# Kernel optimization log

Measured on AMD Instinct MI355X. Metric: run time of the kernel, lower is better.

## Reference

```python
import jax, jax.numpy as jnp
import numpy as np
from jax import lax

MAX_ALPHA = 0.00015
MAX_BETA = 0.00015
NOISE_GRAIN = 0.05
LN_EPS = 1e-5


def gaussian_blur(x, ksize, sigma):
    # depthwise 2D gaussian blur, same padding; x: [B, C, H, W]
    r = ksize // 2
    g = jnp.exp(-(jnp.linspace(-r, r, ksize, dtype=x.dtype) ** 2) / (2.0 * sigma ** 2))
    g = g / g.sum()
    k2d = g[:, None] * g[None, :]                       # [k, k]
    C = x.shape[1]
    kernel = jnp.broadcast_to(k2d, (C, 1, ksize, ksize))  # OIHW, depthwise
    return lax.conv_general_dilated(
        x, kernel, window_strides=(1, 1), padding=[(r, r), (r, r)],
        feature_group_count=C, dimension_numbers=('NCHW', 'OIHW', 'NCHW'))


def setup_inputs() -> dict:
    key = jax.random.key(0)
    ks = jax.random.split(key, 8)
    B, C, H, W = 8, 3, 1024, 1024
    L, D = 1024, 512
    Dh = D // 4
    return {
        'x_bg': jax.random.uniform(ks[0], (B, C, H, W), dtype=jnp.float32),
        'bottleneck_feat': jax.random.normal(ks[1], (B, L, D), dtype=jnp.float32),
        'mask': jax.random.uniform(ks[2], (B, 1, H, W), dtype=jnp.float32),
        'noise': jax.random.normal(ks[3], (B, C, H, W), dtype=jnp.float32),
        'W1': jax.random.normal(ks[4], (D, Dh), dtype=jnp.float32) * (1.0 / np.sqrt(D)),
        'b1': jnp.zeros((Dh,), dtype=jnp.float32),
        'ln_g': jnp.ones((Dh,), dtype=jnp.float32),
        'ln_b': jnp.zeros((Dh,), dtype=jnp.float32),
        'W2': jax.random.normal(ks[5], (Dh, 2), dtype=jnp.float32) * 0.01,
        'b2': jnp.zeros((2,), dtype=jnp.float32),
    }


def reference(x_bg, bottleneck_feat, mask, noise, W1, b1, ln_g, ln_b, W2, b2):
    # param head on global-pooled bottleneck feature
    feat_global = bottleneck_feat.mean(axis=1)                 # [B, D]
    h = feat_global @ W1 + b1                                  # [B, D/4]
    mu = h.mean(axis=-1, keepdims=True)
    var = ((h - mu) ** 2).mean(axis=-1, keepdims=True)
    h = (h - mu) * lax.rsqrt(var + LN_EPS) * ln_g + ln_b
    h = jax.nn.relu(h)
    params = h @ W2 + b2                                       # [B, 2]
    alpha = jax.nn.sigmoid(params[:, 0])[:, None, None, None] * MAX_ALPHA
    beta = jax.nn.sigmoid(params[:, 1])[:, None, None, None] * MAX_BETA

    # synthesize
    variance = alpha * x_bg + beta
    sigma = jnp.sqrt(jnp.maximum(variance, 1e-7))
    n = gaussian_blur(noise, 7, NOISE_GRAIN) * 1.5
    mask_soft = gaussian_blur(mask, 21, 5.0)                   # [B,1,H,W] broadcast
    noisy_output = x_bg + n * sigma * mask_soft
    return noisy_output, alpha, beta
```

## Files before the change

kernel.cpp:

```cpp
#include <hip/hip_runtime.h>
#include <math.h>

#define B 8
#define C 3
#define H 1024
#define W 1024
#define L 1024
#define D 512
#define DH 128
#define NPIX (H * W)
#define NOISY_ELEMS (B * C * NPIX)
#define TH 16

typedef float vf2 __attribute__((ext_vector_type(2)));
typedef float vf4 __attribute__((ext_vector_type(4)));

struct BlurW { float w[21]; };

__global__ __launch_bounds__(256) void hblur_colsum_kernel(
        const float* __restrict__ mask, float* __restrict__ hmask,
        const float* __restrict__ feat, float* __restrict__ partial, BlurW kw) {
    int wgid = blockIdx.x;
    int t = threadIdx.x;
    __shared__ float srow[W + 24];

    if (wgid < 8192) {
        int l = wgid;
        const float* src = mask + (size_t)l * W;
        if (t < 10) { srow[2 + t] = 0.f; srow[12 + W + t] = 0.f; }
        vf4 v = __builtin_nontemporal_load((const vf4*)src + t);
        ((vf4*)(srow + 12))[t] = v;
        __syncthreads();
        float* dst = hmask + (size_t)l * W;
        #pragma unroll
        for (int i = 0; i < 4; ++i) {
            int x = t + 256 * i;
            float acc = 0.f;
            #pragma unroll
            for (int k = 0; k < 10; ++k)
                acc = fmaf(kw.w[k], srow[x + 2 + k] + srow[x + 22 - k], acc);
            acc = fmaf(kw.w[10], srow[x + 12], acc);
            dst[x] = acc;
        }
    } else {
        int blk = wgid - 8192;
        int b = blk >> 6, chunk = blk & 63;
        const float* base = feat + (size_t)b * (L * D) + (size_t)chunk * 16 * D;
        float s0 = 0.f, s1 = 0.f;
        for (int ll = 0; ll < 16; ++ll) {
            s0 += base[ll * D + t];
            s1 += base[ll * D + t + 256];
        }
        float* dst = partial + (size_t)blk * D;
        dst[t] = s0;
        dst[t + 256] = s1;
    }
}

__global__ void head_kernel(const float* __restrict__ partial,
                            const float* __restrict__ W1, const float* __restrict__ b1,
                            const float* __restrict__ ln_g, const float* __restrict__ ln_b,
                            const float* __restrict__ W2, const float* __restrict__ b2,
                            float* __restrict__ ab, float* __restrict__ out_tail) {
    const int b = blockIdx.x;
    const int j = threadIdx.x;
    __shared__ float fm[D];
    __shared__ float red[DH];
    for (int d = j; d < D; d += DH) {
        float s = 0.f;
        const float* p = partial + (size_t)b * 64 * D + d;
        for (int c = 0; c < 64; ++c) s += p[c * D];
        fm[d] = s * (1.0f / (float)L);
    }
    __syncthreads();
    float h = b1[j];
    const vf4* fm4 = (const vf4*)fm;
    #pragma unroll 8
    for (int d4 = 0; d4 < D / 4; ++d4) {
        vf4 f = fm4[d4];
        h = fmaf(f.x, W1[(4 * d4 + 0) * DH + j], h);
        h = fmaf(f.y, W1[(4 * d4 + 1) * DH + j], h);
        h = fmaf(f.z, W1[(4 * d4 + 2) * DH + j], h);
        h = fmaf(f.w, W1[(4 * d4 + 3) * DH + j], h);
    }

    red[j] = h; __syncthreads();
    for (int s = 64; s > 0; s >>= 1) { if (j < s) red[j] += red[j + s]; __syncthreads(); }
    float mu = red[0] * (1.f / (float)DH);
    __syncthreads();
    float hc = h - mu;
    red[j] = hc * hc; __syncthreads();
    for (int s = 64; s > 0; s >>= 1) { if (j < s) red[j] += red[j + s]; __syncthreads(); }
    float var = red[0] * (1.f / (float)DH);
    __syncthreads();

    float hn = hc * rsqrtf(var + 1e-5f) * ln_g[j] + ln_b[j];
    hn = fmaxf(hn, 0.f);

    red[j] = hn * W2[j * 2 + 0]; __syncthreads();
    for (int s = 64; s > 0; s >>= 1) { if (j < s) red[j] += red[j + s]; __syncthreads(); }
    float p0 = red[0];
    __syncthreads();
    red[j] = hn * W2[j * 2 + 1]; __syncthreads();
    for (int s = 64; s > 0; s >>= 1) { if (j < s) red[j] += red[j + s]; __syncthreads(); }
    float p1 = red[0];

    if (j == 0) {
        float a  = 0.00015f / (1.f + expf(-(p0 + b2[0])));
        float be = 0.00015f / (1.f + expf(-(p1 + b2[1])));
        ab[b] = a; ab[8 + b] = be;
        out_tail[b] = a; out_tail[8 + b] = be;
    }
}

__global__ __launch_bounds__(256) void final_kernel(
        const float* __restrict__ x_bg, const float* __restrict__ noise,
        const float* __restrict__ hmask, const float* __restrict__ ab,
        float* __restrict__ out, BlurW kw) {
    int blk = blockIdx.x;
    int b   = blk >> 7;
    int rem = blk & 127;
    int s   = rem >> 1;
    int wj  = rem & 1;
    int h0  = s * TH;
    int t   = threadIdx.x;
    int x0  = wj * 512 + 2 * t;

    const float* hmb = hmask + (size_t)b * NPIX + x0;
    const vf2 zero2 = {0.f, 0.f};

    vf2 win[21];
    #pragma unroll
    for (int k = 0; k < 21; ++k) {
        int hy = h0 - 10 + k;
        win[k] = (hy >= 0 && hy < H) ? *(const vf2*)(hmb + (size_t)hy * W) : zero2;
    }

    float alpha = ab[b], beta = ab[8 + b];

    #pragma unroll
    for (int r = 0; r < TH; ++r) {
        vf2 ms = zero2;
        #pragma unroll
        for (int k = 0; k < 10; ++k) {
            float wk = kw.w[k];
            vf2 v1 = win[(r + k) % 21];
            vf2 v2 = win[(r + 20 - k) % 21];
            ms.x = fmaf(wk, v1.x + v2.x, ms.x);
            ms.y = fmaf(wk, v1.y + v2.y, ms.y);
        }
        {
            vf2 vm = win[(r + 10) % 21];
            ms.x = fmaf(kw.w[10], vm.x, ms.x);
            ms.y = fmaf(kw.w[10], vm.y, ms.y);
        }
        int h = h0 + r;
        #pragma unroll
        for (int c = 0; c < C; ++c) {
            size_t idx = (((size_t)(b * C + c) * H) + h) * W + x0;
            vf2 x = __builtin_nontemporal_load((const vf2*)(x_bg + idx));
            vf2 nz = __builtin_nontemporal_load((const vf2*)(noise + idx));
            vf2 o;
            float sgx = sqrtf(fmaxf(fmaf(alpha, x.x, beta), 1e-7f));
            float sgy = sqrtf(fmaxf(fmaf(alpha, x.y, beta), 1e-7f));
            o.x = fmaf(1.5f * nz.x * sgx, ms.x, x.x);
            o.y = fmaf(1.5f * nz.y * sgy, ms.y, x.y);
            __builtin_nontemporal_store(o, (vf2*)(out + idx));
        }
        if (r < TH - 1) {
            int hy = h0 + r + 11;
            win[r % 21] = (hy < H) ? *(const vf2*)(hmb + (size_t)hy * W) : zero2;
        }
    }
}

extern "C" void kernel_launch(void* const* d_in, const int* in_sizes, int n_in,
                              void* d_out, int out_size, void* d_ws, size_t ws_size,
                              hipStream_t stream) {
    const float* x_bg = (const float*)d_in[0];
    const float* feat = (const float*)d_in[1];
    const float* mask = (const float*)d_in[2];
    const float* noise = (const float*)d_in[3];
    const float* W1 = (const float*)d_in[4];
    const float* b1 = (const float*)d_in[5];
    const float* ln_g = (const float*)d_in[6];
    const float* ln_b = (const float*)d_in[7];
    const float* W2 = (const float*)d_in[8];
    const float* b2 = (const float*)d_in[9];
    float* out = (float*)d_out;

    float* ws_f = (float*)d_ws;
    float* partial = ws_f;
    float* ab = ws_f + 262144;
    float* hmask = ws_f + 262144 + 64;

    BlurW kw;
    {
        double g[21], s = 0.0;
        for (int i = 0; i < 21; ++i) { double x = (double)(i - 10); g[i] = exp(-x * x / 50.0); s += g[i]; }
        for (int i = 0; i < 21; ++i) kw.w[i] = (float)(g[i] / s);
    }

    hblur_colsum_kernel<<<8192 + 512, 256, 0, stream>>>(mask, hmask, feat, partial, kw);
    head_kernel<<<B, 128, 0, stream>>>(partial, W1, b1, ln_g, ln_b, W2, b2,
                                       ab, out + NOISY_ELEMS);
    final_kernel<<<B * 64 * 2, 256, 0, stream>>>(x_bg, noise, hmask, ab, out, kw);
}
```

Baseline: 104.7 us.

## Batch mask rows per block, vectorize blurs, and restructure final kernel accumulation

```diff
diff --git a/kernel.cpp b/kernel.cpp
--- a/kernel.cpp
+++ b/kernel.cpp
@@ -11,6 +11,8 @@
 #define NPIX (H * W)
 #define NOISY_ELEMS (B * C * NPIX)
 #define TH 16
+#define RPB 8
+#define LROW 1056
 
 typedef float vf2 __attribute__((ext_vector_type(2)));
 typedef float vf4 __attribute__((ext_vector_type(4)));
@@ -22,38 +24,57 @@
         const float* __restrict__ feat, float* __restrict__ partial, BlurW kw) {
     int wgid = blockIdx.x;
     int t = threadIdx.x;
-    __shared__ float srow[W + 24];
-
-    if (wgid < 8192) {
-        int l = wgid;
-        const float* src = mask + (size_t)l * W;
-        if (t < 10) { srow[2 + t] = 0.f; srow[12 + W + t] = 0.f; }
-        vf4 v = __builtin_nontemporal_load((const vf4*)src + t);
-        ((vf4*)(srow + 12))[t] = v;
+    __shared__ float Ls[RPB][LROW];
+
+    if (wgid < 1024) {
+        size_t row0 = (size_t)wgid * RPB;
+        const float* src = mask + row0 * W;
+        #pragma unroll
+        for (int r = 0; r < RPB; ++r) {
+            vf4 v = __builtin_nontemporal_load((const vf4*)(src + (size_t)r * W) + t);
+            *(vf4*)&Ls[r][12 + 4 * t] = v;
+        }
+        if (t < RPB * 10) {
+            int r = t / 10, i = t - 10 * r;
+            Ls[r][2 + i] = 0.f;
+            Ls[r][12 + W + i] = 0.f;
+        }
         __syncthreads();
-        float* dst = hmask + (size_t)l * W;
-        #pragma unroll
-        for (int i = 0; i < 4; ++i) {
-            int x = t + 256 * i;
-            float acc = 0.f;
+        float* dst = hmask + row0 * W;
+        #pragma unroll
+        for (int r = 0; r < RPB; ++r) {
+            float v[28];
             #pragma unroll
-            for (int k = 0; k < 10; ++k)
-                acc = fmaf(kw.w[k], srow[x + 2 + k] + srow[x + 22 - k], acc);
-            acc = fmaf(kw.w[10], srow[x + 12], acc);
-            dst[x] = acc;
+            for (int j = 0; j < 7; ++j) {
+                vf4 q = *(const vf4*)&Ls[r][4 * t + 4 * j];
+                v[4 * j] = q.x; v[4 * j + 1] = q.y; v[4 * j + 2] = q.z; v[4 * j + 3] = q.w;
+            }
+            vf4 o;
+            #pragma unroll
+            for (int i = 0; i < 4; ++i) {
+                float acc = 0.f;
+                #pragma unroll
+                for (int k = 0; k < 10; ++k)
+                    acc = fmaf(kw.w[k], v[i + 2 + k] + v[i + 22 - k], acc);
+                o[i] = fmaf(kw.w[10], v[i + 12], acc);
+            }
+            __builtin_nontemporal_store(o, (vf4*)(dst + (size_t)r * W) + t);
         }
     } else {
-        int blk = wgid - 8192;
-        int b = blk >> 6, chunk = blk & 63;
-        const float* base = feat + (size_t)b * (L * D) + (size_t)chunk * 16 * D;
-        float s0 = 0.f, s1 = 0.f;
+        int blk = wgid - 1024;
+        int b = blk >> 5, chunk = blk & 31;
+        int d4 = (t & 127) * 4;
+        int half = t >> 7;
+        const float* base = feat + (size_t)b * (L * D)
+                          + (size_t)(chunk * 32 + half * 16) * D + d4;
+        vf4 s = {0.f, 0.f, 0.f, 0.f};
+        #pragma unroll
         for (int ll = 0; ll < 16; ++ll) {
-            s0 += base[ll * D + t];
-            s1 += base[ll * D + t + 256];
-        }
-        float* dst = partial + (size_t)blk * D;
-        dst[t] = s0;
-        dst[t + 256] = s1;
+            vf4 v = *(const vf4*)(base + (size_t)ll * D);
+            s.x += v.x; s.y += v.y; s.z += v.z; s.w += v.w;
+        }
+        float* dst = partial + ((size_t)(b * 64 + chunk * 2 + half)) * 512 + d4;
+        *(vf4*)dst = s;
     }
 }
 
@@ -129,47 +150,41 @@
     const float* hmb = hmask + (size_t)b * NPIX + x0;
     const vf2 zero2 = {0.f, 0.f};
 
-    vf2 win[21];
+    vf2 ms[TH];
     #pragma unroll
-    for (int k = 0; k < 21; ++k) {
+    for (int r = 0; r < TH; ++r) ms[r] = zero2;
+
+    #pragma unroll
+    for (int k = 0; k < TH + 20; ++k) {
         int hy = h0 - 10 + k;
-        win[k] = (hy >= 0 && hy < H) ? *(const vf2*)(hmb + (size_t)hy * W) : zero2;
+        vf2 wv = (hy >= 0 && hy < H) ? *(const vf2*)(hmb + (size_t)hy * W) : zero2;
+        #pragma unroll
+        for (int r = 0; r < TH; ++r) {
+            int dk = k - r;
+            if (dk >= 0 && dk < 21) {
+                ms[r].x = fmaf(kw.w[dk], wv.x, ms[r].x);
+                ms[r].y = fmaf(kw.w[dk], wv.y, ms[r].y);
+            }
+        }
     }
 
     float alpha = ab[b], beta = ab[8 + b];
 
     #pragma unroll
-    for (int r = 0; r < TH; ++r) {
-        vf2 ms = zero2;
-        #pragma unroll
-        for (int k = 0; k < 10; ++k) {
-            float wk = kw.w[k];
-            vf2 v1 = win[(r + k) % 21];
-            vf2 v2 = win[(r + 20 - k) % 21];
-            ms.x = fmaf(wk, v1.x + v2.x, ms.x);
-            ms.y = fmaf(wk, v1.y + v2.y, ms.y);
-        }
-        {
-            vf2 vm = win[(r + 10) % 21];
-            ms.x = fmaf(kw.w[10], vm.x, ms.x);
-            ms.y = fmaf(kw.w[10], vm.y, ms.y);
-        }
-        int h = h0 + r;
-        #pragma unroll
-        for (int c = 0; c < C; ++c) {
-            size_t idx = (((size_t)(b * C + c) * H) + h) * W + x0;
-            vf2 x = __builtin_nontemporal_load((const vf2*)(x_bg + idx));
-            vf2 nz = __builtin_nontemporal_load((const vf2*)(noise + idx));
+    for (int c = 0; c < C; ++c) {
+        const float* xb = x_bg  + (((size_t)(b * C + c) * H) + h0) * W + x0;
+        const float* nb = noise + (((size_t)(b * C + c) * H) + h0) * W + x0;
+        float*       ob = out   + (((size_t)(b * C + c) * H) + h0) * W + x0;
+        #pragma unroll
+        for (int r = 0; r < TH; ++r) {
+            vf2 x  = __builtin_nontemporal_load((const vf2*)(xb + (size_t)r * W));
+            vf2 nz = __builtin_nontemporal_load((const vf2*)(nb + (size_t)r * W));
             vf2 o;
             float sgx = sqrtf(fmaxf(fmaf(alpha, x.x, beta), 1e-7f));
             float sgy = sqrtf(fmaxf(fmaf(alpha, x.y, beta), 1e-7f));
-            o.x = fmaf(1.5f * nz.x * sgx, ms.x, x.x);
-            o.y = fmaf(1.5f * nz.y * sgy, ms.y, x.y);
-            __builtin_nontemporal_store(o, (vf2*)(out + idx));
-        }
-        if (r < TH - 1) {
-            int hy = h0 + r + 11;
-            win[r % 21] = (hy < H) ? *(const vf2*)(hmb + (size_t)hy * W) : zero2;
+            o.x = fmaf(1.5f * nz.x * sgx, ms[r].x, x.x);
+            o.y = fmaf(1.5f * nz.y * sgy, ms[r].y, x.y);
+            *(vf2*)(ob + (size_t)r * W) = o;
         }
     }
 }
@@ -201,7 +216,7 @@
         for (int i = 0; i < 21; ++i) kw.w[i] = (float)(g[i] / s);
     }
 
-    hblur_colsum_kernel<<<8192 + 512, 256, 0, stream>>>(mask, hmask, feat, partial, kw);
+    hblur_colsum_kernel<<<1024 + 256, 256, 0, stream>>>(mask, hmask, feat, partial, kw);
     head_kernel<<<B, 128, 0, stream>>>(partial, W1, b1, ln_g, ln_b, W2, b2,
                                        ab, out + NOISY_ELEMS);
     final_kernel<<<B * 64 * 2, 256, 0, stream>>>(x_bg, noise, hmask, ab, out, kw);
```

Result: faster. 100.8 us (-3.7%).

## Fuse mask blur into final kernel and merge colsum with head via atomic counter

Applied to the files above, without the earlier changes.

```diff
diff --git a/kernel.cpp b/kernel.cpp
--- a/kernel.cpp
+++ b/kernel.cpp
@@ -17,80 +17,61 @@
 
 struct BlurW { float w[21]; };
 
-__global__ __launch_bounds__(256) void hblur_colsum_kernel(
-        const float* __restrict__ mask, float* __restrict__ hmask,
-        const float* __restrict__ feat, float* __restrict__ partial, BlurW kw) {
-    int wgid = blockIdx.x;
-    int t = threadIdx.x;
-    __shared__ float srow[W + 24];
-
-    if (wgid < 8192) {
-        int l = wgid;
-        const float* src = mask + (size_t)l * W;
-        if (t < 10) { srow[2 + t] = 0.f; srow[12 + W + t] = 0.f; }
-        vf4 v = __builtin_nontemporal_load((const vf4*)src + t);
-        ((vf4*)(srow + 12))[t] = v;
-        __syncthreads();
-        float* dst = hmask + (size_t)l * W;
-        #pragma unroll
-        for (int i = 0; i < 4; ++i) {
-            int x = t + 256 * i;
-            float acc = 0.f;
-            #pragma unroll
-            for (int k = 0; k < 10; ++k)
-                acc = fmaf(kw.w[k], srow[x + 2 + k] + srow[x + 22 - k], acc);
-            acc = fmaf(kw.w[10], srow[x + 12], acc);
-            dst[x] = acc;
-        }
-    } else {
-        int blk = wgid - 8192;
-        int b = blk >> 6, chunk = blk & 63;
-        const float* base = feat + (size_t)b * (L * D) + (size_t)chunk * 16 * D;
-        float s0 = 0.f, s1 = 0.f;
-        for (int ll = 0; ll < 16; ++ll) {
-            s0 += base[ll * D + t];
-            s1 += base[ll * D + t + 256];
-        }
-        float* dst = partial + (size_t)blk * D;
-        dst[t] = s0;
-        dst[t + 256] = s1;
-    }
-}
-
-__global__ void head_kernel(const float* __restrict__ partial,
-                            const float* __restrict__ W1, const float* __restrict__ b1,
-                            const float* __restrict__ ln_g, const float* __restrict__ ln_b,
-                            const float* __restrict__ W2, const float* __restrict__ b2,
-                            float* __restrict__ ab, float* __restrict__ out_tail) {
-    const int b = blockIdx.x;
-    const int j = threadIdx.x;
+__global__ __launch_bounds__(128) void colsum_head_kernel(
+        const float* __restrict__ feat, float* __restrict__ partial,
+        int* __restrict__ counters,
+        const float* __restrict__ W1, const float* __restrict__ b1,
+        const float* __restrict__ ln_g, const float* __restrict__ ln_b,
+        const float* __restrict__ W2, const float* __restrict__ b2,
+        float* __restrict__ ab, float* __restrict__ out_tail) {
+    int blk = blockIdx.x;
+    int b = blk >> 5, chunk = blk & 31;
+    int j = threadIdx.x;
+    int d4 = 4 * j;
+
+    const float* base = feat + (size_t)b * (L * D) + (size_t)chunk * 32 * D + d4;
+    vf4 s = {0.f, 0.f, 0.f, 0.f};
+    #pragma unroll 8
+    for (int ll = 0; ll < 32; ++ll) {
+        vf4 v = *(const vf4*)(base + (size_t)ll * D);
+        s.x += v.x; s.y += v.y; s.z += v.z; s.w += v.w;
+    }
+    *(vf4*)(partial + ((size_t)(b * 32 + chunk)) * 512 + d4) = s;
+
+    __threadfence();
+    __shared__ int winner;
+    if (j == 0) winner = (atomicAdd(&counters[b], 1) == 31);
+    __syncthreads();
+    if (!winner) return;
+    __threadfence();
+
     __shared__ float fm[D];
     __shared__ float red[DH];
     for (int d = j; d < D; d += DH) {
-        float s = 0.f;
-        const float* p = partial + (size_t)b * 64 * D + d;
-        for (int c = 0; c < 64; ++c) s += p[c * D];
-        fm[d] = s * (1.0f / (float)L);
+        float acc = 0.f;
+        const float* p = partial + (size_t)b * 32 * 512 + d;
+        for (int c = 0; c < 32; ++c) acc += p[c * 512];
+        fm[d] = acc * (1.0f / (float)L);
     }
     __syncthreads();
     float h = b1[j];
     const vf4* fm4 = (const vf4*)fm;
     #pragma unroll 8
-    for (int d4 = 0; d4 < D / 4; ++d4) {
-        vf4 f = fm4[d4];
-        h = fmaf(f.x, W1[(4 * d4 + 0) * DH + j], h);
-        h = fmaf(f.y, W1[(4 * d4 + 1) * DH + j], h);
-        h = fmaf(f.z, W1[(4 * d4 + 2) * DH + j], h);
-        h = fmaf(f.w, W1[(4 * d4 + 3) * DH + j], h);
+    for (int q = 0; q < D / 4; ++q) {
+        vf4 f = fm4[q];
+        h = fmaf(f.x, W1[(4 * q + 0) * DH + j], h);
+        h = fmaf(f.y, W1[(4 * q + 1) * DH + j], h);
+        h = fmaf(f.z, W1[(4 * q + 2) * DH + j], h);
+        h = fmaf(f.w, W1[(4 * q + 3) * DH + j], h);
     }
 
     red[j] = h; __syncthreads();
-    for (int s = 64; s > 0; s >>= 1) { if (j < s) red[j] += red[j + s]; __syncthreads(); }
+    for (int st = 64; st > 0; st >>= 1) { if (j < st) red[j] += red[j + st]; __syncthreads(); }
     float mu = red[0] * (1.f / (float)DH);
     __syncthreads();
     float hc = h - mu;
     red[j] = hc * hc; __syncthreads();
-    for (int s = 64; s > 0; s >>= 1) { if (j < s) red[j] += red[j + s]; __syncthreads(); }
+    for (int st = 64; st > 0; st >>= 1) { if (j < st) red[j] += red[j + st]; __syncthreads(); }
     float var = red[0] * (1.f / (float)DH);
     __syncthreads();
 
@@ -98,11 +79,11 @@
     hn = fmaxf(hn, 0.f);
 
     red[j] = hn * W2[j * 2 + 0]; __syncthreads();
-    for (int s = 64; s > 0; s >>= 1) { if (j < s) red[j] += red[j + s]; __syncthreads(); }
+    for (int st = 64; st > 0; st >>= 1) { if (j < st) red[j] += red[j + st]; __syncthreads(); }
     float p0 = red[0];
     __syncthreads();
     red[j] = hn * W2[j * 2 + 1]; __syncthreads();
-    for (int s = 64; s > 0; s >>= 1) { if (j < s) red[j] += red[j + s]; __syncthreads(); }
+    for (int st = 64; st > 0; st >>= 1) { if (j < st) red[j] += red[j + st]; __syncthreads(); }
     float p1 = red[0];
 
     if (j == 0) {
@@ -113,9 +94,9 @@
     }
 }
 
-__global__ __launch_bounds__(256) void final_kernel(
+__global__ __launch_bounds__(256) void mega_kernel(
         const float* __restrict__ x_bg, const float* __restrict__ noise,
-        const float* __restrict__ hmask, const float* __restrict__ ab,
+        const float* __restrict__ mask, const float* __restrict__ ab,
         float* __restrict__ out, BlurW kw) {
     int blk = blockIdx.x;
     int b   = blk >> 7;
@@ -124,52 +105,110 @@
     int wj  = rem & 1;
     int h0  = s * TH;
     int t   = threadIdx.x;
-    int x0  = wj * 512 + 2 * t;
-
-    const float* hmb = hmask + (size_t)b * NPIX + x0;
+    int x0  = wj * 512;
+    bool left = (wj == 0);
+
+    __shared__ float vrow[2][536];
     const vf2 zero2 = {0.f, 0.f};
 
-    vf2 win[21];
+    if (t < 10) {
+        int zi = left ? t : (522 + t);
+        vrow[0][zi] = 0.f;
+        vrow[1][zi] = 0.f;
+    }
+
+    const float* mcol = mask + (size_t)b * NPIX + x0 + 2 * t;
+    vf2 mwin[21];
     #pragma unroll
     for (int k = 0; k < 21; ++k) {
         int hy = h0 - 10 + k;
-        win[k] = (hy >= 0 && hy < H) ? *(const vf2*)(hmb + (size_t)hy * W) : zero2;
+        mwin[k] = (hy >= 0) ? *(const vf2*)(mcol + (size_t)hy * W) : zero2;
+    }
+
+    int hcol_off = left ? (512 + 2 * t) : (502 + 2 * t - 512);
+    const float* hcol = mask + (size_t)b * NPIX + x0 + hcol_off;
+    int hs_i = left ? (522 + 2 * t) : (2 * t);
+    vf2 hwin[21];
+    if (t < 5) {
+        #pragma unroll
+        for (int k = 0; k < 21; ++k) {
+            int hy = h0 - 10 + k;
+            hwin[k] = (hy >= 0) ? *(const vf2*)(hcol + (size_t)hy * W) : zero2;
+        }
     }
 
     float alpha = ab[b], beta = ab[8 + b];
-
-    #pragma unroll
+    int p = 0;
+
     for (int r = 0; r < TH; ++r) {
-        vf2 ms = zero2;
-        #pragma unroll
-        for (int k = 0; k < 10; ++k) {
-            float wk = kw.w[k];
-            vf2 v1 = win[(r + k) % 21];
-            vf2 v2 = win[(r + 20 - k) % 21];
-            ms.x = fmaf(wk, v1.x + v2.x, ms.x);
-            ms.y = fmaf(wk, v1.y + v2.y, ms.y);
-        }
+        int h = h0 + r;
+
+        vf2 vm;
         {
-            vf2 vm = win[(r + 10) % 21];
-            ms.x = fmaf(kw.w[10], vm.x, ms.x);
-            ms.y = fmaf(kw.w[10], vm.y, ms.y);
-        }
-        int h = h0 + r;
+            float ax = 0.f, ay = 0.f;
+            #pragma unroll
+            for (int k = 0; k < 10; ++k) {
+                ax = fmaf(kw.w[k], mwin[k].x + mwin[20 - k].x, ax);
+                ay = fmaf(kw.w[k], mwin[k].y + mwin[20 - k].y, ay);
+            }
+            vm.x = fmaf(kw.w[10], mwin[10].x, ax);
+            vm.y = fmaf(kw.w[10], mwin[10].y, ay);
+        }
+        *(vf2*)&vrow[p][10 + 2 * t] = vm;
+        if (t < 5) {
+            float ax = 0.f, ay = 0.f;
+            #pragma unroll
+            for (int k = 0; k < 10; ++k) {
+                ax = fmaf(kw.w[k], hwin[k].x + hwin[20 - k].x, ax);
+                ay = fmaf(kw.w[k], hwin[k].y + hwin[20 - k].y, ay);
+            }
+            vf2 vh;
+            vh.x = fmaf(kw.w[10], hwin[10].x, ax);
+            vh.y = fmaf(kw.w[10], hwin[10].y, ay);
+            *(vf2*)&vrow[p][hs_i] = vh;
+        }
+        __syncthreads();
+
+        vf2 vv[11];
+        #pragma unroll
+        for (int q = 0; q < 11; ++q) vv[q] = *(const vf2*)&vrow[p][2 * t + 2 * q];
+        float omx = 0.f, omy = 0.f;
+        #pragma unroll
+        for (int q = 0; q < 10; ++q) {
+            float fj  = vv[q >> 1][q & 1];
+            float f20 = vv[(20 - q) >> 1][(20 - q) & 1];
+            float fj1 = vv[(q + 1) >> 1][(q + 1) & 1];
+            float f21 = vv[(21 - q) >> 1][(21 - q) & 1];
+            omx = fmaf(kw.w[q], fj + f20, omx);
+            omy = fmaf(kw.w[q], fj1 + f21, omy);
+        }
+        omx = fmaf(kw.w[10], vv[5].x, omx);
+        omy = fmaf(kw.w[10], vv[5].y, omy);
+
         #pragma unroll
         for (int c = 0; c < C; ++c) {
-            size_t idx = (((size_t)(b * C + c) * H) + h) * W + x0;
-            vf2 x = __builtin_nontemporal_load((const vf2*)(x_bg + idx));
-            vf2 nz = __builtin_nontemporal_load((const vf2*)(noise + idx));
+            size_t idx = (((size_t)(b * C + c) * H) + h) * W + x0 + 2 * t;
+            vf2 x  = *(const vf2*)(x_bg + idx);
+            vf2 nz = *(const vf2*)(noise + idx);
             vf2 o;
             float sgx = sqrtf(fmaxf(fmaf(alpha, x.x, beta), 1e-7f));
             float sgy = sqrtf(fmaxf(fmaf(alpha, x.y, beta), 1e-7f));
-            o.x = fmaf(1.5f * nz.x * sgx, ms.x, x.x);
-            o.y = fmaf(1.5f * nz.y * sgy, ms.y, x.y);
+            o.x = fmaf(1.5f * nz.x * sgx, omx, x.x);
+            o.y = fmaf(1.5f * nz.y * sgy, omy, x.y);
             __builtin_nontemporal_store(o, (vf2*)(out + idx));
         }
+
         if (r < TH - 1) {
             int hy = h0 + r + 11;
-            win[r % 21] = (hy < H) ? *(const vf2*)(hmb + (size_t)hy * W) : zero2;
+            #pragma unroll
+            for (int i = 0; i < 20; ++i) mwin[i] = mwin[i + 1];
+            mwin[20] = (hy < H) ? *(const vf2*)(mcol + (size_t)hy * W) : zero2;
+            if (t < 5) {
+                #pragma unroll
+                for (int i = 0; i < 20; ++i) hwin[i] = hwin[i + 1];
+                hwin[20] = (hy < H) ? *(const vf2*)(hcol + (size_t)hy * W) : zero2;
+            }
+            p ^= 1;
         }
     }
 }
@@ -191,18 +230,19 @@
 
     float* ws_f = (float*)d_ws;
     float* partial = ws_f;
-    float* ab = ws_f + 262144;
-    float* hmask = ws_f + 262144 + 64;
+    float* ab = ws_f + 131072;
+    int* counters = (int*)(ws_f + 131072 + 32);
 
     BlurW kw;
     {
-        double g[21], s = 0.0;
-        for (int i = 0; i < 21; ++i) { double x = (double)(i - 10); g[i] = exp(-x * x / 50.0); s += g[i]; }
-        for (int i = 0; i < 21; ++i) kw.w[i] = (float)(g[i] / s);
-    }
-
-    hblur_colsum_kernel<<<8192 + 512, 256, 0, stream>>>(mask, hmask, feat, partial, kw);
-    head_kernel<<<B, 128, 0, stream>>>(partial, W1, b1, ln_g, ln_b, W2, b2,
-                                       ab, out + NOISY_ELEMS);
-    final_kernel<<<B * 64 * 2, 256, 0, stream>>>(x_bg, noise, hmask, ab, out, kw);
+        double g[21], ssum = 0.0;
+        for (int i = 0; i < 21; ++i) { double x = (double)(i - 10); g[i] = exp(-x * x / 50.0); ssum += g[i]; }
+        for (int i = 0; i < 21; ++i) kw.w[i] = (float)(g[i] / ssum);
+    }
+
+    hipMemsetAsync(counters, 0, 8 * sizeof(int), stream);
+    colsum_head_kernel<<<256, 128, 0, stream>>>(feat, partial, counters,
+                                                W1, b1, ln_g, ln_b, W2, b2,
+                                                ab, out + NOISY_ELEMS);
+    mega_kernel<<<1024, 256, 0, stream>>>(x_bg, noise, mask, ab, out, kw);
 }
```

Result: faster. 100.8 us (-3.7%).
